# Optimization experiments

Measured on AMD Instinct MI355X. Metric: run time of the kernel, lower is better.

The kernel has to match this reference:

```python
import jax, jax.numpy as jnp
import numpy as np

EPS = 1e-8  # torch F.cosine_similarity default eps


def setup_inputs() -> dict:
    key0 = jax.random.key(0)
    k1, k2, k3, k4 = jax.random.split(key0, 4)
    B, H, K, D = 8, 16, 2048, 128
    query = jax.random.normal(k1, (B, H, 1, D), dtype=jnp.float32)
    key = jax.random.normal(k2, (B, H, K, D), dtype=jnp.float32)
    value = jax.random.normal(k3, (B, H, K, D), dtype=jnp.float32)
    mask = jax.random.randint(k4, (B, K), 0, 2, dtype=jnp.int32)
    return {"query": query, "key": key, "value": value, "mask": mask}


def reference(query, key, value, mask):
    # Cosine similarity along the feature dim without materializing the
    # repeated query tensor: broadcast the single query vector per (b, h).
    q_norm = jnp.maximum(jnp.linalg.norm(query, axis=-1), EPS)  # [B, H, 1]
    k_norm = jnp.maximum(jnp.linalg.norm(key, axis=-1), EPS)    # [B, H, K]
    dot = jnp.einsum('bhod,bhkd->bhk', query, key)              # o == 1
    scores = jnp.abs(dot / (q_norm * k_norm))                   # [B, H, K]
    # mask [B, K] -> broadcast over heads; masked positions -> -1e9
    scores = jnp.where(mask[:, None, :] == 0, jnp.float32(-1e9), scores)
    p_attn = jnp.exp(scores)                                    # [B, H, K]
    out = p_attn[:, :, :, None] * value                         # [B, H, K, D]
    return (out, p_attn)
```

## Files before the change

### kernel.cpp

```cpp
#include <hip/hip_runtime.h>
#include <math.h>

#define EPS 1e-8f

constexpr int B = 8, H = 16, K = 2048, D = 128;
constexpr int BH = B * H;
constexpr int SPLIT = 16;
constexpr int ROWS_PER_CHUNK = K / SPLIT;
constexpr int WAVES = 4;
constexpr size_t P_OFF = (size_t)BH * K * D;

__global__ __launch_bounds__(256) void cosattn_kernel(
    const float* __restrict__ q,
    const float* __restrict__ key,
    const float* __restrict__ value,
    const int*   __restrict__ mask,
    float* __restrict__ out)
{
    const int tid  = threadIdx.x;
    const int lane = tid & 63;
    const int half = lane >> 5;
    const int l32  = lane & 31;
    const int wave = tid >> 6;

    const int bh    = blockIdx.x / SPLIT;
    const int chunk = blockIdx.x % SPLIT;
    const int b     = bh / H;

    const float4 qv = *reinterpret_cast<const float4*>(q + (size_t)bh * D + l32 * 4);
    float qsq = qv.x*qv.x + qv.y*qv.y + qv.z*qv.z + qv.w*qv.w;
    #pragma unroll
    for (int s = 16; s >= 1; s >>= 1)
        qsq += __shfl_xor(qsq, s, 64);
    const float qn = fmaxf(sqrtf(qsq), EPS);

    const int row0 = chunk * ROWS_PER_CHUNK;

    #pragma unroll 2
    for (int it = 0; it < ROWS_PER_CHUNK / (WAVES * 2); ++it) {
        const int r = row0 + it * (WAVES * 2) + wave * 2 + half;
        const int mk = mask[b * K + r];
        const size_t rowOff = ((size_t)bh * K + r) * D + l32 * 4;

        float p;
        if (mk != 0) {
            const float4 kv = *reinterpret_cast<const float4*>(key + rowOff);
            float dot = qv.x*kv.x + qv.y*kv.y + qv.z*kv.z + qv.w*kv.w;
            float ksq = kv.x*kv.x + kv.y*kv.y + kv.z*kv.z + kv.w*kv.w;
            #pragma unroll
            for (int s = 16; s >= 1; s >>= 1) {
                dot += __shfl_xor(dot, s, 64);
                ksq += __shfl_xor(ksq, s, 64);
            }
            const float kn = fmaxf(sqrtf(ksq), EPS);
            p = expf(fabsf(dot) / (qn * kn));
            const float4 vv = *reinterpret_cast<const float4*>(value + rowOff);
            float4 ov;
            ov.x = p * vv.x; ov.y = p * vv.y; ov.z = p * vv.z; ov.w = p * vv.w;
            *reinterpret_cast<float4*>(out + rowOff) = ov;
        } else {
            p = 0.0f;
            *reinterpret_cast<float4*>(out + rowOff) = make_float4(0.f, 0.f, 0.f, 0.f);
        }
        if (l32 == 0)
            out[P_OFF + (size_t)bh * K + r] = p;
    }
}

extern "C" void kernel_launch(void* const* d_in, const int* in_sizes, int n_in,
                              void* d_out, int out_size, void* d_ws, size_t ws_size,
                              hipStream_t stream) {
    const float* q   = (const float*)d_in[0];
    const float* key = (const float*)d_in[1];
    const float* val = (const float*)d_in[2];
    const int*   msk = (const int*)d_in[3];
    float* out = (float*)d_out;

    dim3 grid(BH * SPLIT);
    dim3 block(WAVES * 64);
    cosattn_kernel<<<grid, block, 0, stream>>>(q, key, val, msk, out);
}
```

Before: 53.33 us.

## Batch row loads in groups, preload mask via ballot, use nontemporal stores

Each half-wave now loads its whole chunk's mask once and packs it into a bitmask with a ballot, so there is no per-row mask load. Key and value loads for four rows are issued together before the shuffle reductions, which puts more memory requests in flight and interleaves the reductions. Output stores become nontemporal, and the division is replaced by multiplication with reciprocals. The cost is higher register pressure from holding four rows of key and value at once.

```diff
diff --git a/kernel.cpp b/kernel.cpp
--- a/kernel.cpp
+++ b/kernel.cpp
@@ -8,7 +8,13 @@
 constexpr int SPLIT = 16;
 constexpr int ROWS_PER_CHUNK = K / SPLIT;
 constexpr int WAVES = 4;
+constexpr int SLOTS = WAVES * 2;
+constexpr int ROWS_PER_SLOT = ROWS_PER_CHUNK / SLOTS;
+constexpr int GROUP = 4;
+constexpr int NGROUPS = ROWS_PER_SLOT / GROUP;
 constexpr size_t P_OFF = (size_t)BH * K * D;
+
+typedef float f32x4 __attribute__((ext_vector_type(4)));
 
 __global__ __launch_bounds__(256) void cosattn_kernel(
     const float* __restrict__ q,
@@ -22,48 +28,76 @@
     const int half = lane >> 5;
     const int l32  = lane & 31;
     const int wave = tid >> 6;
+    const int slot = wave * 2 + half;
 
     const int bh    = blockIdx.x / SPLIT;
     const int chunk = blockIdx.x % SPLIT;
     const int b     = bh / H;
 
-    const float4 qv = *reinterpret_cast<const float4*>(q + (size_t)bh * D + l32 * 4);
-    float qsq = qv.x*qv.x + qv.y*qv.y + qv.z*qv.z + qv.w*qv.w;
+    const f32x4 qv = *reinterpret_cast<const f32x4*>(q + (size_t)bh * D + l32 * 4);
+    float qsq = qv[0]*qv[0] + qv[1]*qv[1] + qv[2]*qv[2] + qv[3]*qv[3];
     #pragma unroll
     for (int s = 16; s >= 1; s >>= 1)
         qsq += __shfl_xor(qsq, s, 64);
-    const float qn = fmaxf(sqrtf(qsq), EPS);
+    const float inv_qn = 1.0f / fmaxf(sqrtf(qsq), EPS);
 
     const int row0 = chunk * ROWS_PER_CHUNK;
 
-    #pragma unroll 2
-    for (int it = 0; it < ROWS_PER_CHUNK / (WAVES * 2); ++it) {
-        const int r = row0 + it * (WAVES * 2) + wave * 2 + half;
-        const int mk = mask[b * K + r];
-        const size_t rowOff = ((size_t)bh * K + r) * D + l32 * 4;
+    int mk = 0;
+    if (l32 < ROWS_PER_SLOT)
+        mk = mask[b * K + row0 + l32 * SLOTS + slot];
+    const unsigned long long bal = __ballot(mk != 0);
+    const unsigned bits = (unsigned)(bal >> (half * 32)) & 0xFFFFu;
 
-        float p;
-        if (mk != 0) {
-            const float4 kv = *reinterpret_cast<const float4*>(key + rowOff);
-            float dot = qv.x*kv.x + qv.y*kv.y + qv.z*kv.z + qv.w*kv.w;
-            float ksq = kv.x*kv.x + kv.y*kv.y + kv.z*kv.z + kv.w*kv.w;
+    const size_t baseRow = (size_t)bh * K;
+
+    #pragma unroll 1
+    for (int g = 0; g < NGROUPS; ++g) {
+        int   r[GROUP];
+        bool  act[GROUP];
+        f32x4 kv[GROUP], vv[GROUP];
+
+        #pragma unroll
+        for (int j = 0; j < GROUP; ++j) {
+            const int i = g * GROUP + j;
+            r[j]   = row0 + i * SLOTS + slot;
+            act[j] = (bits >> i) & 1u;
+            const size_t off = (baseRow + r[j]) * D + l32 * 4;
+            kv[j] = act[j] ? *reinterpret_cast<const f32x4*>(key + off)
+                           : (f32x4)(0.0f);
+            vv[j] = act[j] ? *reinterpret_cast<const f32x4*>(value + off)
+                           : (f32x4)(0.0f);
+        }
+
+        float dot[GROUP], ksq[GROUP];
+        #pragma unroll
+        for (int j = 0; j < GROUP; ++j) {
+            dot[j] = qv[0]*kv[j][0] + qv[1]*kv[j][1] + qv[2]*kv[j][2] + qv[3]*kv[j][3];
+            ksq[j] = kv[j][0]*kv[j][0] + kv[j][1]*kv[j][1] + kv[j][2]*kv[j][2] + kv[j][3]*kv[j][3];
+        }
+        #pragma unroll
+        for (int s = 16; s >= 1; s >>= 1) {
             #pragma unroll
-            for (int s = 16; s >= 1; s >>= 1) {
-                dot += __shfl_xor(dot, s, 64);
-                ksq += __shfl_xor(ksq, s, 64);
+            for (int j = 0; j < GROUP; ++j) {
+                dot[j] += __shfl_xor(dot[j], s, 64);
+                ksq[j] += __shfl_xor(ksq[j], s, 64);
             }
-            const float kn = fmaxf(sqrtf(ksq), EPS);
-            p = expf(fabsf(dot) / (qn * kn));
-            const float4 vv = *reinterpret_cast<const float4*>(value + rowOff);
-            float4 ov;
-            ov.x = p * vv.x; ov.y = p * vv.y; ov.z = p * vv.z; ov.w = p * vv.w;
-            *reinterpret_cast<float4*>(out + rowOff) = ov;
-        } else {
-            p = 0.0f;
-            *reinterpret_cast<float4*>(out + rowOff) = make_float4(0.f, 0.f, 0.f, 0.f);
         }
-        if (l32 == 0)
-            out[P_OFF + (size_t)bh * K + r] = p;
+
+        #pragma unroll
+        for (int j = 0; j < GROUP; ++j) {
+            const float kn_inv = 1.0f / fmaxf(sqrtf(ksq[j]), EPS);
+            const float p = act[j] ? expf(fabsf(dot[j]) * inv_qn * kn_inv) : 0.0f;
+            f32x4 ov;
+            ov[0] = p * vv[j][0];
+            ov[1] = p * vv[j][1];
+            ov[2] = p * vv[j][2];
+            ov[3] = p * vv[j][3];
+            const size_t off = (baseRow + r[j]) * D + l32 * 4;
+            __builtin_nontemporal_store(ov, reinterpret_cast<f32x4*>(out + off));
+            if (l32 == 0)
+                __builtin_nontemporal_store(p, out + P_OFF + baseRow + r[j]);
+        }
     }
 }
 
```

Measured after the change: 45.44 us. 1.17x faster.
